# Kernel optimization log

Hardware: AMD Instinct MI355X
Metric: run time of the kernel (lower is better)

The kernel has to match this reference:

```python
import jax, jax.numpy as jnp
import numpy as np
import math

D_MODEL = 256  # projected q/k dim
D_K_IN = 32    # raw key feature dim
D_V = 64       # value projection dim
KEEP_PROB = 0.8  # dropout p=0.2

def setup_inputs() -> dict:
    key = jax.random.key(0)
    ks = jax.random.split(key, 9)
    B, Lq, Lk = 4, 4096, 4096
    s = 0.02
    return {
        "q": jax.random.normal(ks[0], (B, Lq, D_MODEL), jnp.float32),
        "k": jax.random.normal(ks[1], (B, Lk, D_K_IN), jnp.float32),
        "v": jax.random.normal(ks[2], (B, Lk, D_MODEL), jnp.float32),
        "Wq": jax.random.normal(ks[3], (D_MODEL, D_MODEL), jnp.float32) * s,
        "bq": jnp.zeros((D_MODEL,), jnp.float32),
        "Wk": jax.random.normal(ks[4], (D_K_IN, D_MODEL), jnp.float32) * s,
        "bk": jnp.zeros((D_MODEL,), jnp.float32),
        "Wv": jax.random.normal(ks[5], (D_MODEL, D_V), jnp.float32) * s,
        "bv": jnp.zeros((D_V,), jnp.float32),
    }

def reference(q, k, v, Wq, bq, Wk, bk, Wv, bv):
    # Linear projections
    qp = q @ Wq + bq                       # [B, Lq, 256]
    kp = k @ Wk + bk                       # [B, Lk, 256]
    vp = v @ Wv + bv                       # [B, Lk, 64]
    scale = 1.0 / math.sqrt(qp.shape[-1])
    scores = jnp.einsum("bqd,bkd->bqk", qp, kp) * scale  # [B, Lq, Lk]
    attn = jax.nn.softmax(scores, axis=-1)
    # dropout p=0.2 (training mode), deterministic key
    mask = jax.random.bernoulli(jax.random.key(42), KEEP_PROB, attn.shape)
    attn = jnp.where(mask, attn / KEEP_PROB, 0.0)
    return jnp.einsum("bqk,bkd->bqd", attn, vp)  # [B, Lq, 64]
```

## Files before the change

### kernel.cpp

```cpp
#include <hip/hip_runtime.h>


typedef short s16x8 __attribute__((ext_vector_type(8)));
typedef float f32x4 __attribute__((ext_vector_type(4)));

#define L    4096
#define DM   256
#define DV   64
#define MTOT 16384
#define KSPLIT 4
#define KBLK 32

__device__ __forceinline__ short f2bf(float f) {
  unsigned u = __builtin_bit_cast(unsigned, f);
  u += 0x7FFFu + ((u >> 16) & 1u);
  return (short)(u >> 16);
}

__device__ __forceinline__ unsigned rotl32c(unsigned x, int r) {
  return (x << r) | (x >> (32 - r));
}

__device__ __forceinline__ unsigned tf_keep(unsigned ctr) {
  unsigned x0 = 0u;
  unsigned x1 = ctr + 42u;
#define TFR(r) { x0 += x1; x1 = rotl32c(x1, r); x1 ^= x0; }
  TFR(13) TFR(15) TFR(26) TFR(6)
  x0 += 42u;          x1 += 0x1BD11BF1u;
  TFR(17) TFR(29) TFR(16) TFR(24)
  x0 += 0x1BD11BF0u;  x1 += 2u;
  TFR(13) TFR(15) TFR(26) TFR(6)
         x1 += 45u;
  TFR(17) TFR(29) TFR(16) TFR(24)
  x0 += 42u;          x1 += 0x1BD11BF4u;
  TFR(13) TFR(15) TFR(26) TFR(6)
  x0 += 0x1BD11BF0u;  x1 += 5u;
#undef TFR
  return ((x0 ^ x1) < 3435974144u) ? 1u : 0u;
}

__global__ __launch_bounds__(256) void prep_kernel(
    const float* __restrict__ Wq, const float* __restrict__ Wk,
    const float* __restrict__ Wv, short* __restrict__ wqT,
    short* __restrict__ wkT, short* __restrict__ wvT) {
  const int idx = blockIdx.x * 256 + threadIdx.x;
  if (idx < 65536) {
    const int n = idx >> 8, k = idx & 255;
    wqT[idx] = f2bf(Wq[k * 256 + n]);
  }
  if (idx < 8192) {
    const int n = idx >> 5, k = idx & 31;
    wkT[idx] = f2bf(Wk[k * 256 + n]);
  }
  if (idx < 16384) {
    const int n = idx >> 8, k = idx & 255;
    wvT[idx] = f2bf(Wv[k * 64 + n]);
  }
}

template <int K, int N, bool TRANS_OUT>
__global__ __launch_bounds__(256) void proj_kernel(
    const float* __restrict__ A, const short* __restrict__ WT,
    const float* __restrict__ bias, short* __restrict__ out) {
  const int lane = threadIdx.x & 63;
  const int wv   = threadIdx.x >> 6;
  const int l15 = lane & 15, l4 = lane >> 4;
  const int rowbase = blockIdx.x * 64 + wv * 16;
  constexpr int NT = N / 16;
  constexpr int KC = K / 32;
  f32x4 acc[NT];
#pragma unroll
  for (int i = 0; i < NT; ++i) acc[i] = (f32x4){0.f, 0.f, 0.f, 0.f};
  const int arow = rowbase + l15;
#pragma unroll
  for (int kc = 0; kc < KC; ++kc) {
    const f32x4* ap = (const f32x4*)(A + (size_t)arow * K + kc * 32 + l4 * 8);
    f32x4 a0 = ap[0], a1 = ap[1];
    s16x8 af;
#pragma unroll
    for (int j = 0; j < 4; ++j) { af[j] = f2bf(a0[j]); af[4 + j] = f2bf(a1[j]); }
#pragma unroll
    for (int nt = 0; nt < NT; ++nt) {
      const s16x8 bf = *(const s16x8*)(WT + (size_t)(nt * 16 + l15) * K + kc * 32 + l4 * 8);
      acc[nt] = __builtin_amdgcn_mfma_f32_16x16x32_bf16(af, bf, acc[nt], 0, 0, 0);
    }
  }
#pragma unroll
  for (int nt = 0; nt < NT; ++nt) {
    const int gcol = nt * 16 + l15;
    const float bv = bias[gcol];
#pragma unroll
    for (int j = 0; j < 4; ++j) {
      const int grow = rowbase + l4 * 4 + j;
      const float vv = acc[nt][j] + bv;
      if (TRANS_OUT) {
        const int b = grow >> 12, key = grow & 4095;
        out[(size_t)(b * 64 + gcol) * L + key] = f2bf(vv);
      } else {
        out[(size_t)grow * N + gcol] = f2bf(vv);
      }
    }
  }
}

__global__ __launch_bounds__(256, 4) void attn_kernel(
    const short* __restrict__ qp, const short* __restrict__ kp,
    const short* __restrict__ vpT, float* __restrict__ partO,
    float* __restrict__ partZ) {
  __shared__ __align__(16) short kbuf[KBLK * 256];
  __shared__ __align__(16) short vbuf[64 * KBLK];
  __shared__ __align__(16) short pbuf[4][16 * KBLK];
  const int tid = threadIdx.x;
  const int lane = tid & 63, wv = tid >> 6;
  const int l15 = lane & 15, l4 = lane >> 4;
  const int qt = blockIdx.x, b = blockIdx.y, z = blockIdx.z;
  const int qrow0 = b * L + qt * 64 + wv * 16;

  s16x8 qf[8];
#pragma unroll
  for (int kc = 0; kc < 8; ++kc)
    qf[kc] = *(const s16x8*)(qp + (size_t)(qrow0 + l15) * DM + kc * 32 + l4 * 8);

  f32x4 accO[4];
#pragma unroll
  for (int i = 0; i < 4; ++i) accO[i] = (f32x4){0.f, 0.f, 0.f, 0.f};
  float zpart[4] = {0.f, 0.f, 0.f, 0.f};

  const unsigned qglob = (unsigned)qrow0;
  constexpr float CEXP = 0.09016844005556021f;
  const int kb0 = z * (L / KSPLIT / KBLK);

  for (int i = 0; i < L / KSPLIT / KBLK; ++i) {
    const int kbase = (kb0 + i) * KBLK;
    __syncthreads();
    {
      const short* src = kp + (size_t)(b * L + kbase) * DM;
#pragma unroll
      for (int it = 0; it < 4; ++it) {
        const int c = it * 256 + tid;
        const int row = c >> 5, off = (c & 31) * 8;
        const int e = (row * 256 + off) ^ ((row & 7) << 3);
        *(s16x8*)(kbuf + e) = *(const s16x8*)(src + (size_t)row * DM + off);
      }
      const short* vsrc = vpT + (size_t)b * 64 * L + kbase;
      const int row = tid >> 2, off = (tid & 3) * 8;
      const int e = (row * KBLK + off) ^ ((row & 3) << 3);
      *(s16x8*)(vbuf + e) = *(const s16x8*)(vsrc + (size_t)row * L + off);
    }
    __syncthreads();

    f32x4 sf[2];
#pragma unroll
    for (int kt = 0; kt < 2; ++kt) sf[kt] = (f32x4){0.f, 0.f, 0.f, 0.f};
#pragma unroll
    for (int kc = 0; kc < 8; ++kc) {
#pragma unroll
      for (int kt = 0; kt < 2; ++kt) {
        const int row = kt * 16 + l15;
        const int e = (row * 256 + kc * 32 + l4 * 8) ^ ((row & 7) << 3);
        const s16x8 kf = *(const s16x8*)(kbuf + e);
        sf[kt] = __builtin_amdgcn_mfma_f32_16x16x32_bf16(qf[kc], kf, sf[kt], 0, 0, 0);
      }
    }

    unsigned keep = 0;
#pragma unroll
    for (int kt = 0; kt < 2; ++kt) {
#pragma unroll
      for (int j = 0; j < 4; ++j) {
        const unsigned q = qglob + (unsigned)(l4 * 4 + j);
        const unsigned idx = (q << 12) + (unsigned)(kbase + kt * 16 + l15);
        keep |= tf_keep(idx) << (kt * 4 + j);
      }
    }

#pragma unroll
    for (int kt = 0; kt < 2; ++kt) {
#pragma unroll
      for (int j = 0; j < 4; ++j) {
        const float e = exp2f(sf[kt][j] * CEXP);
        zpart[j] += e;
        const float pd = ((keep >> (kt * 4 + j)) & 1u) ? e : 0.0f;
        const int row = l4 * 4 + j, col = kt * 16 + l15;
        const int pe = (row * KBLK + col) ^ ((row & 3) << 3);
        pbuf[wv][pe] = f2bf(pd);
      }
    }
    __syncthreads();

    {
      const int pe = (l15 * KBLK + l4 * 8) ^ ((l15 & 3) << 3);
      const s16x8 pa = *(const s16x8*)(&pbuf[wv][0] + pe);
#pragma unroll
      for (int nt = 0; nt < 4; ++nt) {
        const int vrow = nt * 16 + l15;
        const int ve = (vrow * KBLK + l4 * 8) ^ ((vrow & 3) << 3);
        const s16x8 vb = *(const s16x8*)(vbuf + ve);
        accO[nt] = __builtin_amdgcn_mfma_f32_16x16x32_bf16(pa, vb, accO[nt], 0, 0, 0);
      }
    }
  }

#pragma unroll
  for (int j = 0; j < 4; ++j) {
    float zf = zpart[j];
    zf += __shfl_xor(zf, 1);
    zf += __shfl_xor(zf, 2);
    zf += __shfl_xor(zf, 4);
    zf += __shfl_xor(zf, 8);
    const int grow = qrow0 + l4 * 4 + j;
    if (l15 == 0) partZ[(size_t)z * MTOT + grow] = zf;
#pragma unroll
    for (int nt = 0; nt < 4; ++nt)
      partO[((size_t)z * MTOT + grow) * DV + nt * 16 + l15] = accO[nt][j];
  }
}

__global__ __launch_bounds__(256) void combine_kernel(
    const float* __restrict__ partO, const float* __restrict__ partZ,
    float* __restrict__ out) {
  const int i = blockIdx.x * 256 + threadIdx.x;
  const int row = i >> 4;
  f32x4 acc = (f32x4){0.f, 0.f, 0.f, 0.f};
  float zf = 0.f;
#pragma unroll
  for (int zz = 0; zz < KSPLIT; ++zz) {
    acc += *(const f32x4*)(partO + (size_t)zz * MTOT * DV + (size_t)i * 4);
    zf += partZ[(size_t)zz * MTOT + row];
  }
  const float inv = 1.0f / (0.8f * zf);
  f32x4 r = acc * inv;
  *(f32x4*)(out + (size_t)i * 4) = r;
}

extern "C" void kernel_launch(void* const* d_in, const int* in_sizes, int n_in,
                              void* d_out, int out_size, void* d_ws, size_t ws_size,
                              hipStream_t stream) {
  const float* q  = (const float*)d_in[0];
  const float* k  = (const float*)d_in[1];
  const float* v  = (const float*)d_in[2];
  const float* Wq = (const float*)d_in[3];
  const float* bq = (const float*)d_in[4];
  const float* Wk = (const float*)d_in[5];
  const float* bk = (const float*)d_in[6];
  const float* Wv = (const float*)d_in[7];
  const float* bv = (const float*)d_in[8];
  float* out = (float*)d_out;

  short* qp  = (short*)d_ws;
  short* kpb = qp + (size_t)MTOT * DM;
  short* vpT = kpb + (size_t)MTOT * DM;
  float* partO = (float*)(vpT + (size_t)4 * 64 * L);
  float* partZ = partO + (size_t)KSPLIT * MTOT * DV;
  short* wqT = (short*)(partZ + (size_t)KSPLIT * MTOT);
  short* wkT = wqT + 256 * 256;
  short* wvT = wkT + 32 * 256;

  prep_kernel<<<352, 256, 0, stream>>>(Wq, Wk, Wv, wqT, wkT, wvT);
  proj_kernel<256, 256, false><<<MTOT / 64, 256, 0, stream>>>(q, wqT, bq, qp);
  proj_kernel<32, 256, false><<<MTOT / 64, 256, 0, stream>>>(k, wkT, bk, kpb);
  proj_kernel<256, 64, true><<<MTOT / 64, 256, 0, stream>>>(v, wvT, bv, vpT);
  attn_kernel<<<dim3(64, 4, KSPLIT), 256, 0, stream>>>(qp, kpb, vpT, partO, partZ);
  combine_kernel<<<MTOT * DV / 1024, 256, 0, stream>>>(partO, partZ, out);
}
```

Baseline: 364.1 us.

## Raise key split, fold softmax scale into Wq, bf16 partials, column-split projections

```diff
diff --git a/kernel.cpp b/kernel.cpp
--- a/kernel.cpp
+++ b/kernel.cpp
@@ -2,26 +2,31 @@
 
 
 typedef short s16x8 __attribute__((ext_vector_type(8)));
+typedef short s16x4 __attribute__((ext_vector_type(4)));
 typedef float f32x4 __attribute__((ext_vector_type(4)));
 
 #define L    4096
 #define DM   256
 #define DV   64
 #define MTOT 16384
-#define KSPLIT 4
+#define KSPLIT 8
 #define KBLK 32
+#define CEXP 0.09016844005556021f
 
 __device__ __forceinline__ short f2bf(float f) {
   unsigned u = __builtin_bit_cast(unsigned, f);
   u += 0x7FFFu + ((u >> 16) & 1u);
   return (short)(u >> 16);
 }
-
+__device__ __forceinline__ float bf2f(short s) {
+  unsigned u = ((unsigned)(unsigned short)s) << 16;
+  return __builtin_bit_cast(float, u);
+}
 __device__ __forceinline__ unsigned rotl32c(unsigned x, int r) {
   return (x << r) | (x >> (32 - r));
 }
 
-__device__ __forceinline__ unsigned tf_keep(unsigned ctr) {
+__device__ __forceinline__ unsigned tf_bits(unsigned ctr) {
   unsigned x0 = 0u;
   unsigned x1 = ctr + 42u;
 #define TFR(r) { x0 += x1; x1 = rotl32c(x1, r); x1 ^= x0; }
@@ -36,17 +41,18 @@
   TFR(13) TFR(15) TFR(26) TFR(6)
   x0 += 0x1BD11BF0u;  x1 += 5u;
 #undef TFR
-  return ((x0 ^ x1) < 3435974144u) ? 1u : 0u;
+  return x0 ^ x1;
 }
 
 __global__ __launch_bounds__(256) void prep_kernel(
-    const float* __restrict__ Wq, const float* __restrict__ Wk,
-    const float* __restrict__ Wv, short* __restrict__ wqT,
-    short* __restrict__ wkT, short* __restrict__ wvT) {
+    const float* __restrict__ Wq, const float* __restrict__ bq,
+    const float* __restrict__ Wk, const float* __restrict__ Wv,
+    short* __restrict__ wqT, short* __restrict__ wkT,
+    short* __restrict__ wvT, float* __restrict__ bqs) {
   const int idx = blockIdx.x * 256 + threadIdx.x;
   if (idx < 65536) {
     const int n = idx >> 8, k = idx & 255;
-    wqT[idx] = f2bf(Wq[k * 256 + n]);
+    wqT[idx] = f2bf(Wq[k * 256 + n] * CEXP);
   }
   if (idx < 8192) {
     const int n = idx >> 5, k = idx & 31;
@@ -56,9 +62,10 @@
     const int n = idx >> 8, k = idx & 255;
     wvT[idx] = f2bf(Wv[k * 64 + n]);
   }
-}
-
-template <int K, int N, bool TRANS_OUT>
+  if (idx < 256) bqs[idx] = bq[idx] * CEXP;
+}
+
+template <int K, int NOUT>
 __global__ __launch_bounds__(256) void proj_kernel(
     const float* __restrict__ A, const short* __restrict__ WT,
     const float* __restrict__ bias, short* __restrict__ out) {
@@ -66,49 +73,42 @@
   const int wv   = threadIdx.x >> 6;
   const int l15 = lane & 15, l4 = lane >> 4;
   const int rowbase = blockIdx.x * 64 + wv * 16;
-  constexpr int NT = N / 16;
-  constexpr int KC = K / 32;
-  f32x4 acc[NT];
-#pragma unroll
-  for (int i = 0; i < NT; ++i) acc[i] = (f32x4){0.f, 0.f, 0.f, 0.f};
+  const int ncol0 = blockIdx.y * 64;
+  f32x4 acc[4];
+#pragma unroll
+  for (int i = 0; i < 4; ++i) acc[i] = (f32x4){0.f, 0.f, 0.f, 0.f};
   const int arow = rowbase + l15;
 #pragma unroll
-  for (int kc = 0; kc < KC; ++kc) {
+  for (int kc = 0; kc < K / 32; ++kc) {
     const f32x4* ap = (const f32x4*)(A + (size_t)arow * K + kc * 32 + l4 * 8);
     f32x4 a0 = ap[0], a1 = ap[1];
     s16x8 af;
 #pragma unroll
     for (int j = 0; j < 4; ++j) { af[j] = f2bf(a0[j]); af[4 + j] = f2bf(a1[j]); }
 #pragma unroll
-    for (int nt = 0; nt < NT; ++nt) {
-      const s16x8 bf = *(const s16x8*)(WT + (size_t)(nt * 16 + l15) * K + kc * 32 + l4 * 8);
+    for (int nt = 0; nt < 4; ++nt) {
+      const s16x8 bf = *(const s16x8*)(WT + (size_t)(ncol0 + nt * 16 + l15) * K + kc * 32 + l4 * 8);
       acc[nt] = __builtin_amdgcn_mfma_f32_16x16x32_bf16(af, bf, acc[nt], 0, 0, 0);
     }
   }
 #pragma unroll
-  for (int nt = 0; nt < NT; ++nt) {
-    const int gcol = nt * 16 + l15;
+  for (int nt = 0; nt < 4; ++nt) {
+    const int gcol = ncol0 + nt * 16 + l15;
     const float bv = bias[gcol];
 #pragma unroll
     for (int j = 0; j < 4; ++j) {
       const int grow = rowbase + l4 * 4 + j;
-      const float vv = acc[nt][j] + bv;
-      if (TRANS_OUT) {
-        const int b = grow >> 12, key = grow & 4095;
-        out[(size_t)(b * 64 + gcol) * L + key] = f2bf(vv);
-      } else {
-        out[(size_t)grow * N + gcol] = f2bf(vv);
-      }
-    }
-  }
-}
-
-__global__ __launch_bounds__(256, 4) void attn_kernel(
+      out[(size_t)grow * NOUT + gcol] = f2bf(acc[nt][j] + bv);
+    }
+  }
+}
+
+__global__ __launch_bounds__(256, 6) void attn_kernel(
     const short* __restrict__ qp, const short* __restrict__ kp,
-    const short* __restrict__ vpT, float* __restrict__ partO,
+    const short* __restrict__ vp, short* __restrict__ partO,
     float* __restrict__ partZ) {
   __shared__ __align__(16) short kbuf[KBLK * 256];
-  __shared__ __align__(16) short vbuf[64 * KBLK];
+  __shared__ __align__(16) short vbuf[DV * KBLK];
   __shared__ __align__(16) short pbuf[4][16 * KBLK];
   const int tid = threadIdx.x;
   const int lane = tid & 63, wv = tid >> 6;
@@ -127,11 +127,10 @@
   float zpart[4] = {0.f, 0.f, 0.f, 0.f};
 
   const unsigned qglob = (unsigned)qrow0;
-  constexpr float CEXP = 0.09016844005556021f;
-  const int kb0 = z * (L / KSPLIT / KBLK);
+  const int vkey = tid & 31, vdv0 = (tid >> 5) * 8;
 
   for (int i = 0; i < L / KSPLIT / KBLK; ++i) {
-    const int kbase = (kb0 + i) * KBLK;
+    const int kbase = (z * (L / KSPLIT / KBLK) + i) * KBLK;
     __syncthreads();
     {
       const short* src = kp + (size_t)(b * L + kbase) * DM;
@@ -142,10 +141,12 @@
         const int e = (row * 256 + off) ^ ((row & 7) << 3);
         *(s16x8*)(kbuf + e) = *(const s16x8*)(src + (size_t)row * DM + off);
       }
-      const short* vsrc = vpT + (size_t)b * 64 * L + kbase;
-      const int row = tid >> 2, off = (tid & 3) * 8;
-      const int e = (row * KBLK + off) ^ ((row & 3) << 3);
-      *(s16x8*)(vbuf + e) = *(const s16x8*)(vsrc + (size_t)row * L + off);
+      const s16x8 vv = *(const s16x8*)(vp + (size_t)(b * L + kbase + vkey) * DV + vdv0);
+#pragma unroll
+      for (int m = 0; m < 8; ++m) {
+        const int dv = vdv0 + m;
+        vbuf[dv * KBLK + (vkey ^ ((dv & 3) << 3))] = vv[m];
+      }
     }
     __syncthreads();
 
@@ -163,27 +164,17 @@
       }
     }
 
-    unsigned keep = 0;
 #pragma unroll
     for (int kt = 0; kt < 2; ++kt) {
 #pragma unroll
       for (int j = 0; j < 4; ++j) {
-        const unsigned q = qglob + (unsigned)(l4 * 4 + j);
-        const unsigned idx = (q << 12) + (unsigned)(kbase + kt * 16 + l15);
-        keep |= tf_keep(idx) << (kt * 4 + j);
-      }
-    }
-
-#pragma unroll
-    for (int kt = 0; kt < 2; ++kt) {
-#pragma unroll
-      for (int j = 0; j < 4; ++j) {
-        const float e = exp2f(sf[kt][j] * CEXP);
+        const float e = exp2f(sf[kt][j]);
         zpart[j] += e;
-        const float pd = ((keep >> (kt * 4 + j)) & 1u) ? e : 0.0f;
+        const unsigned idx = ((qglob + (unsigned)(l4 * 4 + j)) << 12) +
+                             (unsigned)(kbase + kt * 16 + l15);
+        const float pd = (tf_bits(idx) < 3435974144u) ? e : 0.0f;
         const int row = l4 * 4 + j, col = kt * 16 + l15;
-        const int pe = (row * KBLK + col) ^ ((row & 3) << 3);
-        pbuf[wv][pe] = f2bf(pd);
+        pbuf[wv][(row * KBLK + col) ^ ((row & 3) << 3)] = f2bf(pd);
       }
     }
     __syncthreads();
@@ -212,25 +203,26 @@
     if (l15 == 0) partZ[(size_t)z * MTOT + grow] = zf;
 #pragma unroll
     for (int nt = 0; nt < 4; ++nt)
-      partO[((size_t)z * MTOT + grow) * DV + nt * 16 + l15] = accO[nt][j];
+      partO[((size_t)z * MTOT + grow) * DV + nt * 16 + l15] = f2bf(accO[nt][j]);
   }
 }
 
 __global__ __launch_bounds__(256) void combine_kernel(
-    const float* __restrict__ partO, const float* __restrict__ partZ,
+    const short* __restrict__ partO, const float* __restrict__ partZ,
     float* __restrict__ out) {
   const int i = blockIdx.x * 256 + threadIdx.x;
-  const int row = i >> 4;
+  const int row = i >> 4, col0 = (i & 15) * 4;
   f32x4 acc = (f32x4){0.f, 0.f, 0.f, 0.f};
   float zf = 0.f;
 #pragma unroll
-  for (int zz = 0; zz < KSPLIT; ++zz) {
-    acc += *(const f32x4*)(partO + (size_t)zz * MTOT * DV + (size_t)i * 4);
-    zf += partZ[(size_t)zz * MTOT + row];
+  for (int z = 0; z < KSPLIT; ++z) {
+    const s16x4 p = *(const s16x4*)(partO + (((size_t)z * MTOT + row) << 6) + col0);
+#pragma unroll
+    for (int m = 0; m < 4; ++m) acc[m] += bf2f(p[m]);
+    zf += partZ[(size_t)z * MTOT + row];
   }
   const float inv = 1.0f / (0.8f * zf);
-  f32x4 r = acc * inv;
-  *(f32x4*)(out + (size_t)i * 4) = r;
+  *(f32x4*)(out + (size_t)i * 4) = acc * inv;
 }
 
 extern "C" void kernel_launch(void* const* d_in, const int* in_sizes, int n_in,
@@ -249,17 +241,18 @@
 
   short* qp  = (short*)d_ws;
   short* kpb = qp + (size_t)MTOT * DM;
-  short* vpT = kpb + (size_t)MTOT * DM;
-  float* partO = (float*)(vpT + (size_t)4 * 64 * L);
-  float* partZ = partO + (size_t)KSPLIT * MTOT * DV;
+  short* vp  = kpb + (size_t)MTOT * DM;
+  short* partO = vp + (size_t)MTOT * DV;
+  float* partZ = (float*)(partO + (size_t)KSPLIT * MTOT * DV);
   short* wqT = (short*)(partZ + (size_t)KSPLIT * MTOT);
   short* wkT = wqT + 256 * 256;
   short* wvT = wkT + 32 * 256;
-
-  prep_kernel<<<352, 256, 0, stream>>>(Wq, Wk, Wv, wqT, wkT, wvT);
-  proj_kernel<256, 256, false><<<MTOT / 64, 256, 0, stream>>>(q, wqT, bq, qp);
-  proj_kernel<32, 256, false><<<MTOT / 64, 256, 0, stream>>>(k, wkT, bk, kpb);
-  proj_kernel<256, 64, true><<<MTOT / 64, 256, 0, stream>>>(v, wvT, bv, vpT);
-  attn_kernel<<<dim3(64, 4, KSPLIT), 256, 0, stream>>>(qp, kpb, vpT, partO, partZ);
+  float* bqs = (float*)(wvT + 64 * 256);
+
+  prep_kernel<<<256, 256, 0, stream>>>(Wq, bq, Wk, Wv, wqT, wkT, wvT, bqs);
+  proj_kernel<256, 256><<<dim3(MTOT / 64, 4), 256, 0, stream>>>(q, wqT, bqs, qp);
+  proj_kernel<32, 256><<<dim3(MTOT / 64, 4), 256, 0, stream>>>(k, wkT, bk, kpb);
+  proj_kernel<256, 64><<<dim3(MTOT / 64, 1), 256, 0, stream>>>(v, wvT, bv, vp);
+  attn_kernel<<<dim3(64, 4, KSPLIT), 256, 0, stream>>>(qp, kpb, vp, partO, partZ);
   combine_kernel<<<MTOT * DV / 1024, 256, 0, stream>>>(partO, partZ, out);
 }
```

Result: slower. 465.1 us (+27.8%).
